# Kernel tuning notes

Hardware: AMD Instinct MI355X
Metric: run time of the kernel (lower is better)

The kernel has to match this reference:

```python
import jax, jax.numpy as jnp
import numpy as np
import math
from jax import lax

ROT = math.radians(45.0)   # rotation_range in radians
TR = 1.0                   # translation_range
P = 50                     # n_particles
ITERS = 30                 # n_iterations
SUB = 256                  # fitness_subsample
MU = P // 2
C_SIGMA = 0.3
D_SIGMA = 1.0


def axis_angle_to_R(a):
    # a: [..., 3] -> [..., 3, 3] via Rodrigues' formula
    theta = jnp.linalg.norm(a, axis=-1, keepdims=True)
    axis = a / (theta + 1e-8)
    x, y, z = axis[..., 0], axis[..., 1], axis[..., 2]
    o = jnp.zeros_like(x)
    K = jnp.stack([jnp.stack([o, -z, y], -1),
                   jnp.stack([z, o, -x], -1),
                   jnp.stack([-y, x, o], -1)], -2)
    th = theta[..., None]
    I = jnp.eye(3, dtype=a.dtype)
    return I + jnp.sin(th) * K + (1.0 - jnp.cos(th)) * (K @ K)


def chamfer(x, y):
    # x: [M,S,3], y: [M,T,3] -> [M]; symmetric chamfer on squared NN distances
    d2 = (jnp.sum(x * x, -1)[:, :, None] + jnp.sum(y * y, -1)[:, None, :]
          - 2.0 * jnp.einsum('msd,mtd->mst', x, y))
    return jnp.min(d2, axis=2).mean(axis=1) + jnp.min(d2, axis=1).mean(axis=1)


def evaluate(src, tgt, positions):
    # src [B,S,3], tgt [B,T,3], positions [B,Pn,6] -> fitness [B,Pn]
    B, Pn, _ = positions.shape
    R = axis_angle_to_R(positions[..., :3])            # [B,Pn,3,3]
    t = positions[..., 3:]
    transformed = jnp.einsum('bnj,bpkj->bpnk', src, R) + t[:, :, None, :]
    x = transformed.reshape(B * Pn, -1, 3)
    y = jnp.broadcast_to(tgt[:, None], (B, Pn) + tgt.shape[1:]).reshape(B * Pn, -1, 3)
    return chamfer(x, y).reshape(B, Pn)


def clamp6(v):
    return jnp.concatenate([jnp.clip(v[..., :3], -ROT, ROT),
                            jnp.clip(v[..., 3:], -TR, TR)], axis=-1)


def run_cmaes(source, target, key):
    B, N, _ = source.shape
    M = target.shape[1]
    S = min(SUB, N)
    k1, k2, k3 = jax.random.split(key, 3)
    src = source[:, jax.random.permutation(k1, N)[:S], :] if S < N else source
    tgt = target[:, jax.random.permutation(k2, M)[:S], :] if S < M else target

    mean = jnp.zeros((B, 6), jnp.float32)
    sigma = jnp.concatenate([jnp.full((B, 3), ROT * 0.3, jnp.float32),
                             jnp.full((B, 3), TR * 0.3, jnp.float32)], axis=1)
    w = np.log(MU + 0.5) - np.log(np.arange(1, MU + 1))
    w = jnp.asarray(w / w.sum(), jnp.float32)       # [MU] recombination weights
    gbest_pos = mean
    gbest_fit = jnp.full((B,), jnp.inf, jnp.float32)

    def step(carry, k):
        mean, sigma, gbest_pos, gbest_fit = carry
        z = jax.random.normal(k, (B, P, 6), jnp.float32)
        off = clamp6(mean[:, None] + sigma[:, None] * z)        # [B,P,6]
        fit = evaluate(src, tgt, off)                            # [B,P]
        order = jnp.argsort(fit, axis=1)
        pidx = order[:, :MU]
        pz = jnp.take_along_axis(z, pidx[..., None], axis=1)     # [B,MU,6]
        ppos = jnp.take_along_axis(off, pidx[..., None], axis=1)
        mean_new = jnp.einsum('m,bmd->bd', w, ppos)
        mean_z = jnp.einsum('m,bmd->bd', w, pz)
        s = sigma * jnp.exp(C_SIGMA / D_SIGMA * (jnp.mean(jnp.abs(mean_z), -1, keepdims=True) - 1.0))
        s = jnp.concatenate([jnp.clip(s[:, :3], ROT * 0.01, ROT * 0.5),
                             jnp.clip(s[:, 3:], TR * 0.01, TR * 0.5)], axis=1)
        best_fit = jnp.take_along_axis(fit, order[:, :1], axis=1)[:, 0]
        best_pos = jnp.take_along_axis(off, order[:, :1, None], axis=1)[:, 0]
        impr = best_fit < gbest_fit
        gbest_pos = jnp.where(impr[:, None], best_pos, gbest_pos)
        gbest_fit = jnp.where(impr, best_fit, gbest_fit)
        return (mean_new, s, gbest_pos, gbest_fit), None

    keys = jax.random.split(k3, ITERS)
    (mean, sigma, gbest_pos, gbest_fit), _ = lax.scan(step, (mean, sigma, gbest_pos, gbest_fit), keys)

    mean_fit = evaluate(src, tgt, mean[:, None, :])[:, 0]
    gbest_pos = jnp.where((mean_fit < gbest_fit)[:, None], mean, gbest_pos)
    return gbest_pos


def _forward(source, target):
    # Optimization runs under no_grad in the original -> stop_gradient here
    gbest = lax.stop_gradient(run_cmaes(source, target, jax.random.key(42)))
    R = axis_angle_to_R(gbest[:, :3])          # [B,3,3]
    t = gbest[:, 3:]                            # [B,3]
    aligned = jnp.einsum('bnj,bkj->bnk', source, R) + t[:, None, :]
    return R, t, aligned


def setup_inputs() -> dict:
    key = jax.random.key(0)
    k1, k2 = jax.random.split(key)
    source = jax.random.normal(k1, (32, 16384, 3), jnp.float32)
    target = jax.random.normal(k2, (32, 16384, 3), jnp.float32)
    return {"source": source, "target": target}


def reference(source, target):
    return _forward(source, target)
```

## Files before the change

### kernel.cpp

```cpp
#include <hip/hip_runtime.h>
#include <stdint.h>
#include <math.h>

#define NB 32
#define NPTS 16384
#define SS 256
#define POPP 50
#define MUU 25
#define NITERS 30

#define ROTF  ((float)0.7853981633974483)
#define SIG0R ((float)(0.7853981633974483*0.3))
#define SIG0T ((float)0.3)
#define SLOR  ((float)(0.7853981633974483*0.01))
#define SHIR  ((float)(0.7853981633974483*0.5))
#define SLOT  ((float)0.01)
#define SHIT  ((float)0.5)
#define SQRT2F ((float)1.4142135623730951)
#define ULOW  (-0.99999994f)

__host__ __device__ inline uint32_t rotl32(uint32_t v, int n){ return (v<<n)|(v>>(32-n)); }

__host__ __device__ inline void tf2x32(uint32_t k0, uint32_t k1, uint32_t x0, uint32_t x1,
                                       uint32_t &o0, uint32_t &o1){
  uint32_t ks2 = k0 ^ k1 ^ 0x1BD11BDAu;
  x0 += k0; x1 += k1;
#define TFR(r) { x0 += x1; x1 = rotl32(x1, r); x1 ^= x0; }
  TFR(13) TFR(15) TFR(26) TFR(6)
  x0 += k1; x1 += ks2 + 1u;
  TFR(17) TFR(29) TFR(16) TFR(24)
  x0 += ks2; x1 += k0 + 2u;
  TFR(13) TFR(15) TFR(26) TFR(6)
  x0 += k0; x1 += k1 + 3u;
  TFR(17) TFR(29) TFR(16) TFR(24)
  x0 += k1; x1 += ks2 + 4u;
  TFR(13) TFR(15) TFR(26) TFR(6)
  x0 += ks2; x1 += k0 + 5u;
#undef TFR
  o0 = x0; o1 = x1;
}

__device__ inline float erfinv32(float x){
  float w = -log1pf(-x*x);
  float p;
  if (w < 5.0f) {
    w = w - 2.5f;
    p = 2.81022636e-08f;
    p = fmaf(p, w, 3.43273939e-07f);
    p = fmaf(p, w, -3.5233877e-06f);
    p = fmaf(p, w, -4.39150654e-06f);
    p = fmaf(p, w, 0.00021858087f);
    p = fmaf(p, w, -0.00125372503f);
    p = fmaf(p, w, -0.00417768164f);
    p = fmaf(p, w, 0.246640727f);
    p = fmaf(p, w, 1.50140941f);
  } else {
    w = sqrtf(w) - 3.0f;
    p = -0.000200214257f;
    p = fmaf(p, w, 0.000100950558f);
    p = fmaf(p, w, 0.00134934322f);
    p = fmaf(p, w, -0.00367342844f);
    p = fmaf(p, w, 0.00573950773f);
    p = fmaf(p, w, -0.0076224613f);
    p = fmaf(p, w, 0.00943887047f);
    p = fmaf(p, w, 1.00167406f);
    p = fmaf(p, w, 2.83297682f);
  }
  return p * x;
}

__device__ inline void axisangle_R(float ax, float ay, float az, float R[9]){
  float th = sqrtf(ax*ax + ay*ay + az*az);
  float den = th + 1e-8f;
  float ux = ax/den, uy = ay/den, uz = az/den;
  float s = sinf(th), c = cosf(th);
  float omc = 1.0f - c;
  float xx=ux*ux, yy=uy*uy, zz=uz*uz;
  float xy=ux*uy, xz=ux*uz, yz=uy*uz;
  R[0] = 1.0f + omc*(-(yy+zz));
  R[1] = s*(-uz) + omc*xy;
  R[2] = s*uy    + omc*xz;
  R[3] = s*uz    + omc*xy;
  R[4] = 1.0f + omc*(-(xx+zz));
  R[5] = s*(-ux) + omc*yz;
  R[6] = s*(-uy) + omc*xz;
  R[7] = s*ux    + omc*yz;
  R[8] = 1.0f + omc*(-(xx+yy));
}

struct WArr { float w[MUU]; };

__global__ void k_init(float* mean, float* sigma, float* gbest_pos, float* gbest_fit){
  int i = blockIdx.x*blockDim.x + threadIdx.x;
  if (i < NB*6){
    mean[i] = 0.0f;
    gbest_pos[i] = 0.0f;
    int d = i % 6;
    sigma[i] = (d < 3) ? SIG0R : SIG0T;
  }
  if (i < NB) gbest_fit[i] = INFINITY;
}

__global__ void k_genperm(uint64_t* comp, uint32_t sa0, uint32_t sa1,
                          uint32_t sb0, uint32_t sb1, int round){
  int i = blockIdx.x*blockDim.x + threadIdx.x;
  if (i >= 2*NPTS) return;
  int a = i >> 14;
  int idx = i & (NPTS-1);
  uint32_t kk0 = a ? sb0 : sa0;
  uint32_t kk1 = a ? sb1 : sa1;
  uint32_t o0,o1; tf2x32(kk0, kk1, 0u, (uint32_t)idx, o0, o1);
  uint32_t key = o0 ^ o1;
  uint64_t val = (round == 0) ? (uint64_t)idx : (comp[i] & 0x3FFFull);
  comp[i] = ((uint64_t)key << 28) | ((uint64_t)idx << 14) | val;
}

__global__ __launch_bounds__(1024) void k_sort_local(uint64_t* comp){
  __shared__ uint64_t buf[4096];
  int c = blockIdx.x;
  int base = c * 4096;
  int abase = (c & 3) * 4096;
  for (int t = threadIdx.x; t < 4096; t += 1024) buf[t] = comp[base + t];
  __syncthreads();
  for (int k = 2; k <= 4096; k <<= 1){
    for (int j = k >> 1; j > 0; j >>= 1){
      for (int idx = threadIdx.x; idx < 2048; idx += 1024){
        int i = ((idx & ~(j-1)) << 1) | (idx & (j-1));
        int pi = i | j;
        bool dir = (((abase + i) & k) == 0);
        uint64_t A = buf[i], Bv = buf[pi];
        bool sw = dir ? (A > Bv) : (A < Bv);
        if (sw){ buf[i] = Bv; buf[pi] = A; }
      }
      __syncthreads();
    }
  }
  for (int t = threadIdx.x; t < 4096; t += 1024) comp[base + t] = buf[t];
}

__global__ void k_sort_global(uint64_t* comp, int k, int j){
  int t = blockIdx.x*blockDim.x + threadIdx.x;
  if (t >= NPTS) return;
  int a = t >> 13;
  int idx = t & 8191;
  int i = ((idx & ~(j-1)) << 1) | (idx & (j-1));
  int pi = i | j;
  bool dir = ((i & k) == 0);
  uint64_t* arr = comp + (size_t)a * NPTS;
  uint64_t A = arr[i], Bv = arr[pi];
  bool sw = dir ? (A > Bv) : (A < Bv);
  if (sw){ arr[i] = Bv; arr[pi] = A; }
}

__global__ __launch_bounds__(1024) void k_sort_finish(uint64_t* comp, int k){
  __shared__ uint64_t buf[4096];
  int c = blockIdx.x;
  int base = c * 4096;
  int abase = (c & 3) * 4096;
  for (int t = threadIdx.x; t < 4096; t += 1024) buf[t] = comp[base + t];
  __syncthreads();
  for (int j = 2048; j > 0; j >>= 1){
    for (int idx = threadIdx.x; idx < 2048; idx += 1024){
      int i = ((idx & ~(j-1)) << 1) | (idx & (j-1));
      int pi = i | j;
      bool dir = (((abase + i) & k) == 0);
      uint64_t A = buf[i], Bv = buf[pi];
      bool sw = dir ? (A > Bv) : (A < Bv);
      if (sw){ buf[i] = Bv; buf[pi] = A; }
    }
    __syncthreads();
  }
  for (int t = threadIdx.x; t < 4096; t += 1024) comp[base + t] = buf[t];
}

__global__ void k_gather(const uint64_t* comp, const float* source, const float* target,
                         float* src_sub, float* tgt_sub){
  int t = blockIdx.x*blockDim.x + threadIdx.x;
  if (t >= 2*NB*SS) return;
  int a = t / (NB*SS);
  int r = t % (NB*SS);
  int b = r / SS;
  int s2 = r % SS;
  int val = (int)(comp[(size_t)a*NPTS + s2] & 0x3FFFull);
  const float* inp = a ? target : source;
  float* outp = a ? tgt_sub : src_sub;
  for (int d = 0; d < 3; ++d)
    outp[((size_t)b*SS + s2)*3 + d] = inp[((size_t)b*NPTS + val)*3 + d];
}

__global__ __launch_bounds__(256) void k_se(uint32_t ka, uint32_t kb,
    const float* __restrict__ mean, const float* __restrict__ sigma,
    const float* __restrict__ src_sub, const float* __restrict__ tgt_sub,
    float* __restrict__ z_buf, float* __restrict__ off_buf,
    float* __restrict__ fit){
  int c = blockIdx.x;
  int b = c / POPP;
  int tid = threadIdx.x;
  int wave = tid >> 6;
  int lane = tid & 63;
  __shared__ float qoff[6];
  __shared__ float4 ysd[SS];
  __shared__ float4 xsd[SS];
  __shared__ float rmp[4][SS];
  __shared__ float cmp[4][SS];
  __shared__ float wpart[4];

  if (tid < 6){
    int i = c*6 + tid;
    uint32_t o0,o1; tf2x32(ka, kb, 0u, (uint32_t)i, o0, o1);
    uint32_t bits = o0 ^ o1;
    float u = __uint_as_float((bits >> 9) | 0x3F800000u) - 1.0f;
    u = u * 2.0f + ULOW;
    u = fmaxf(ULOW, u);
    float zz = SQRT2F * erfinv32(u);
    float m = mean[b*6 + tid], sg = sigma[b*6 + tid];
    float v = fmaf(sg, zz, m);
    float lim = (tid < 3) ? ROTF : 1.0f;
    v = fminf(fmaxf(v, -lim), lim);
    z_buf[i] = zz; off_buf[i] = v; qoff[tid] = v;
  }
  __syncthreads();

  float R[9];
  axisangle_R(qoff[0], qoff[1], qoff[2], R);
  float tx=qoff[3], ty=qoff[4], tz=qoff[5];

  {
    const float* tp = tgt_sub + ((size_t)b*SS + tid)*3;
    float Y0=tp[0], Y1=tp[1], Y2=tp[2];
    float sy = fmaf(Y2,Y2, fmaf(Y1,Y1, Y0*Y0));
    ysd[tid] = make_float4(-2.0f*Y0, -2.0f*Y1, -2.0f*Y2, sy);
  }
  {
    const float* sp = src_sub + ((size_t)b*SS + tid)*3;
    float X0=sp[0], X1=sp[1], X2=sp[2];
    float px = fmaf(X2, R[2], fmaf(X1, R[1], X0*R[0])) + tx;
    float py = fmaf(X2, R[5], fmaf(X1, R[4], X0*R[3])) + ty;
    float pz = fmaf(X2, R[8], fmaf(X1, R[7], X0*R[6])) + tz;
    float sx = fmaf(pz,pz, fmaf(py,py, px*px));
    xsd[tid] = make_float4(-2.0f*px, -2.0f*py, -2.0f*pz, sx);
  }
  __syncthreads();

  float pxj[4],pyj[4],pzj[4];
  float yxj[4],yyj[4],yzj[4];
  #pragma unroll
  for (int j = 0; j < 4; ++j){
    int i = lane + 64*j;
    float4 xv = xsd[i];
    pxj[j] = -0.5f*xv.x; pyj[j] = -0.5f*xv.y; pzj[j] = -0.5f*xv.z;
    float4 yv = ysd[i];
    yxj[j] = -0.5f*yv.x; yyj[j] = -0.5f*yv.y; yzj[j] = -0.5f*yv.z;
  }

  float rm0=INFINITY, rm1=INFINITY, rm2=INFINITY, rm3=INFINITY;
  float cm0=INFINITY, cm1=INFINITY, cm2=INFINITY, cm3=INFINITY;
  int tbeg = wave*64;
  #pragma unroll 8
  for (int t = tbeg; t < tbeg+64; ++t){
    float4 yv = ysd[t];
    float4 xv = xsd[t];
    rm0 = fminf(rm0, fmaf(pxj[0], yv.x, fmaf(pyj[0], yv.y, fmaf(pzj[0], yv.z, yv.w))));
    rm1 = fminf(rm1, fmaf(pxj[1], yv.x, fmaf(pyj[1], yv.y, fmaf(pzj[1], yv.z, yv.w))));
    rm2 = fminf(rm2, fmaf(pxj[2], yv.x, fmaf(pyj[2], yv.y, fmaf(pzj[2], yv.z, yv.w))));
    rm3 = fminf(rm3, fmaf(pxj[3], yv.x, fmaf(pyj[3], yv.y, fmaf(pzj[3], yv.z, yv.w))));
    cm0 = fminf(cm0, fmaf(yxj[0], xv.x, fmaf(yyj[0], xv.y, fmaf(yzj[0], xv.z, xv.w))));
    cm1 = fminf(cm1, fmaf(yxj[1], xv.x, fmaf(yyj[1], xv.y, fmaf(yzj[1], xv.z, xv.w))));
    cm2 = fminf(cm2, fmaf(yxj[2], xv.x, fmaf(yyj[2], xv.y, fmaf(yzj[2], xv.z, xv.w))));
    cm3 = fminf(cm3, fmaf(yxj[3], xv.x, fmaf(yyj[3], xv.y, fmaf(yzj[3], xv.z, xv.w))));
  }

  rmp[wave][lane+  0] = rm0;  cmp[wave][lane+  0] = cm0;
  rmp[wave][lane+ 64] = rm1;  cmp[wave][lane+ 64] = cm1;
  rmp[wave][lane+128] = rm2;  cmp[wave][lane+128] = cm2;
  rmp[wave][lane+192] = rm3;  cmp[wave][lane+192] = cm3;
  __syncthreads();

  float fx = xsd[tid].w + fminf(fminf(rmp[0][tid], rmp[1][tid]),
                                fminf(rmp[2][tid], rmp[3][tid]));
  float fy = ysd[tid].w + fminf(fminf(cmp[0][tid], cmp[1][tid]),
                                fminf(cmp[2][tid], cmp[3][tid]));
  float acc = fx + fy;

  for (int m = 32; m > 0; m >>= 1) acc += __shfl_xor(acc, m, 64);
  if (lane == 0) wpart[wave] = acc;
  __syncthreads();
  if (tid == 0) fit[c] = (((wpart[0]+wpart[1])+wpart[2])+wpart[3]) * (1.0f/256.0f);
}

__global__ __launch_bounds__(128) void k_eval(const float* __restrict__ pos, int Pn,
    const float* __restrict__ src_sub, const float* __restrict__ tgt_sub,
    float* __restrict__ fit){
  int c = blockIdx.x;
  int b = c / Pn;
  int tid = threadIdx.x;
  int wave = tid >> 6;
  int lane = tid & 63;
  __shared__ float4 ysd[SS];
  __shared__ float4 xsd[SS];
  __shared__ float wpart[2];

  const float* q = pos + (size_t)c*6;
  float R[9];
  axisangle_R(q[0], q[1], q[2], R);
  float tx=q[3], ty=q[4], tz=q[5];

  for (int i = tid; i < SS; i += 128){
    const float* tp = tgt_sub + ((size_t)b*SS + i)*3;
    float Y0=tp[0], Y1=tp[1], Y2=tp[2];
    float sy = fmaf(Y2,Y2, fmaf(Y1,Y1, Y0*Y0));
    ysd[i] = make_float4(-2.0f*Y0, -2.0f*Y1, -2.0f*Y2, sy);
  }

  int xi0 = wave*128 + lane;
  int xi1 = xi0 + 64;
  float px0,py0,pz0,sx0, px1,py1,pz1,sx1;
  {
    const float* sp = src_sub + ((size_t)b*SS + xi0)*3;
    float X0=sp[0], X1=sp[1], X2=sp[2];
    px0 = fmaf(X2, R[2], fmaf(X1, R[1], X0*R[0])) + tx;
    py0 = fmaf(X2, R[5], fmaf(X1, R[4], X0*R[3])) + ty;
    pz0 = fmaf(X2, R[8], fmaf(X1, R[7], X0*R[6])) + tz;
    sx0 = fmaf(pz0,pz0, fmaf(py0,py0, px0*px0));
    xsd[xi0] = make_float4(-2.0f*px0, -2.0f*py0, -2.0f*pz0, sx0);
  }
  {
    const float* sp = src_sub + ((size_t)b*SS + xi1)*3;
    float X0=sp[0], X1=sp[1], X2=sp[2];
    px1 = fmaf(X2, R[2], fmaf(X1, R[1], X0*R[0])) + tx;
    py1 = fmaf(X2, R[5], fmaf(X1, R[4], X0*R[3])) + ty;
    pz1 = fmaf(X2, R[8], fmaf(X1, R[7], X0*R[6])) + tz;
    sx1 = fmaf(pz1,pz1, fmaf(py1,py1, px1*px1));
    xsd[xi1] = make_float4(-2.0f*px1, -2.0f*py1, -2.0f*pz1, sx1);
  }
  __syncthreads();

  float rm0 = INFINITY, rm1 = INFINITY;
  #pragma unroll 8
  for (int t = 0; t < SS; ++t){
    float4 yv = ysd[t];
    rm0 = fminf(rm0, fmaf(px0, yv.x, fmaf(py0, yv.y, fmaf(pz0, yv.z, yv.w))));
    rm1 = fminf(rm1, fmaf(px1, yv.x, fmaf(py1, yv.y, fmaf(pz1, yv.z, yv.w))));
  }
  float acc = (sx0 + rm0) + (sx1 + rm1);

  float4 yv0 = ysd[xi0];
  float4 yv1 = ysd[xi1];
  float yx0 = -0.5f*yv0.x, yy0 = -0.5f*yv0.y, yz0 = -0.5f*yv0.z, sy0 = yv0.w;
  float yx1 = -0.5f*yv1.x, yy1 = -0.5f*yv1.y, yz1 = -0.5f*yv1.z, sy1 = yv1.w;
  float cm0 = INFINITY, cm1 = INFINITY;
  #pragma unroll 8
  for (int t = 0; t < SS; ++t){
    float4 xv = xsd[t];
    cm0 = fminf(cm0, fmaf(yx0, xv.x, fmaf(yy0, xv.y, fmaf(yz0, xv.z, xv.w))));
    cm1 = fminf(cm1, fmaf(yx1, xv.x, fmaf(yy1, xv.y, fmaf(yz1, xv.z, xv.w))));
  }
  acc += (sy0 + cm0) + (sy1 + cm1);

  for (int m = 32; m > 0; m >>= 1) acc += __shfl_xor(acc, m, 64);
  if (lane == 0) wpart[wave] = acc;
  __syncthreads();
  if (tid == 0) fit[c] = (wpart[0] + wpart[1]) * (1.0f/256.0f);
}

__global__ __launch_bounds__(64) void k_update(const float* __restrict__ fit,
    const float* __restrict__ off, const float* __restrict__ z,
    float* mean, float* sigma, float* gbest_pos, float* gbest_fit, WArr W){
  int b = blockIdx.x;
  int tid = threadIdx.x;
  __shared__ float lfit[POPP];
  __shared__ int order[POPP];
  __shared__ float mn[6], mz[6];
  if (tid < POPP) lfit[tid] = fit[b*POPP + tid];
  __syncthreads();
  if (tid < POPP){
    float f = lfit[tid];
    int r = 0;
    for (int j = 0; j < POPP; ++j){
      float fj = lfit[j];
      r += (fj < f) || (fj == f && j < tid);
    }
    order[r] = tid;
  }
  __syncthreads();
  if (tid < 6){
    float a = 0.0f, bz = 0.0f;
    for (int m = 0; m < MUU; ++m){
      int idx = order[m];
      a  = fmaf(W.w[m], off[((size_t)b*POPP + idx)*6 + tid], a);
      bz = fmaf(W.w[m], z  [((size_t)b*POPP + idx)*6 + tid], bz);
    }
    mn[tid] = a; mz[tid] = bz;
  }
  __syncthreads();
  if (tid == 0){
    float avg = (((((fabsf(mz[0])+fabsf(mz[1]))+fabsf(mz[2]))+fabsf(mz[3]))+fabsf(mz[4]))+fabsf(mz[5])) / 6.0f;
    float e = expf(0.3f * (avg - 1.0f));
    for (int d = 0; d < 6; ++d){
      float sN = sigma[b*6 + d] * e;
      float lo = (d < 3) ? SLOR : SLOT;
      float hi = (d < 3) ? SHIR : SHIT;
      sN = fminf(fmaxf(sN, lo), hi);
      sigma[b*6 + d] = sN;
      mean[b*6 + d] = mn[d];
    }
    int i0 = order[0];
    float bf = lfit[i0];
    if (bf < gbest_fit[b]){
      gbest_fit[b] = bf;
      for (int d = 0; d < 6; ++d) gbest_pos[b*6 + d] = off[((size_t)b*POPP + i0)*6 + d];
    }
  }
}

__global__ void k_finalize(const float* mean, const float* mean_fit,
                           const float* gbest_pos, const float* gbest_fit, float* out){
  int b = blockIdx.x;
  if (threadIdx.x != 0) return;
  bool um = mean_fit[b] < gbest_fit[b];
  float g[6];
  for (int d = 0; d < 6; ++d) g[d] = um ? mean[b*6 + d] : gbest_pos[b*6 + d];
  float R[9];
  axisangle_R(g[0], g[1], g[2], R);
  for (int i = 0; i < 9; ++i) out[b*9 + i] = R[i];
  for (int d = 0; d < 3; ++d) out[NB*9 + b*3 + d] = g[3 + d];
}

__global__ void k_aligned(const float* __restrict__ src, const float* __restrict__ out_rt,
                          float* __restrict__ aligned){
  int idx = blockIdx.x*blockDim.x + threadIdx.x;
  if (idx >= NB*NPTS) return;
  int b = idx / NPTS;
  const float* R = out_rt + b*9;
  const float* t = out_rt + NB*9 + b*3;
  const float* p = src + (size_t)idx*3;
  float X0=p[0], X1=p[1], X2=p[2];
  float* o = aligned + (size_t)idx*3;
  o[0] = fmaf(X2, R[2], fmaf(X1, R[1], X0*R[0])) + t[0];
  o[1] = fmaf(X2, R[5], fmaf(X1, R[4], X0*R[3])) + t[1];
  o[2] = fmaf(X2, R[8], fmaf(X1, R[7], X0*R[6])) + t[2];
}

struct HKey { uint32_t a, b; };
static inline HKey h_tf(HKey k, uint32_t x0, uint32_t x1){
  uint32_t o0,o1; tf2x32(k.a, k.b, x0, x1, o0, o1);
  return {o0, o1};
}

static void run_sort(uint64_t* comp, hipStream_t stream){
  hipLaunchKernelGGL(k_sort_local,  dim3(8),  dim3(1024), 0, stream, comp);
  hipLaunchKernelGGL(k_sort_global, dim3(64), dim3(256),  0, stream, comp, 8192, 4096);
  hipLaunchKernelGGL(k_sort_finish, dim3(8),  dim3(1024), 0, stream, comp, 8192);
  hipLaunchKernelGGL(k_sort_global, dim3(64), dim3(256),  0, stream, comp, 16384, 8192);
  hipLaunchKernelGGL(k_sort_global, dim3(64), dim3(256),  0, stream, comp, 16384, 4096);
  hipLaunchKernelGGL(k_sort_finish, dim3(8),  dim3(1024), 0, stream, comp, 16384);
}

extern "C" void kernel_launch(void* const* d_in, const int* in_sizes, int n_in,
                              void* d_out, int out_size, void* d_ws, size_t ws_size,
                              hipStream_t stream){
  const float* source = (const float*)d_in[0];
  const float* target = (const float*)d_in[1];
  float* out = (float*)d_out;

  uint8_t* w = (uint8_t*)d_ws;
  size_t o = 0;
  auto alloc = [&](size_t bytes){ void* p = w + o; o += (bytes + 255) & ~(size_t)255; return p; };
  uint64_t* comp   = (uint64_t*)alloc(2*(size_t)NPTS*8);
  float* src_sub   = (float*)alloc((size_t)NB*SS*3*4);
  float* tgt_sub   = (float*)alloc((size_t)NB*SS*3*4);
  float* z_buf     = (float*)alloc((size_t)NB*POPP*6*4);
  float* off_buf   = (float*)alloc((size_t)NB*POPP*6*4);
  float* fit_buf   = (float*)alloc((size_t)NB*POPP*4);
  float* mean_buf  = (float*)alloc((size_t)NB*6*4);
  float* sigma_buf = (float*)alloc((size_t)NB*6*4);
  float* gb_pos    = (float*)alloc((size_t)NB*6*4);
  float* gb_fit    = (float*)alloc((size_t)NB*4);
  float* mean_fit  = (float*)alloc((size_t)NB*4);
  (void)ws_size; (void)in_sizes; (void)n_in; (void)out_size;

  HKey key0 = {0u, 42u};
  HKey k1 = h_tf(key0, 0u, 0u);
  HKey k2 = h_tf(key0, 0u, 1u);
  HKey k3 = h_tf(key0, 0u, 2u);
  HKey srcA  = h_tf(k1, 0u, 0u);
  HKey srcS1 = h_tf(k1, 0u, 1u);
  HKey srcS2 = h_tf(srcA, 0u, 1u);
  HKey tgtA  = h_tf(k2, 0u, 0u);
  HKey tgtS1 = h_tf(k2, 0u, 1u);
  HKey tgtS2 = h_tf(tgtA, 0u, 1u);
  HKey itk[NITERS];
  for (int j = 0; j < NITERS; ++j) itk[j] = h_tf(k3, 0u, (uint32_t)j);

  WArr W;
  {
    double lw[MUU], s = 0.0;
    for (int m = 0; m < MUU; ++m){ lw[m] = log((double)MUU + 0.5) - log((double)(m+1)); s += lw[m]; }
    for (int m = 0; m < MUU; ++m) W.w[m] = (float)(lw[m] / s);
  }

  hipLaunchKernelGGL(k_init, dim3(1), dim3(256), 0, stream, mean_buf, sigma_buf, gb_pos, gb_fit);

  hipLaunchKernelGGL(k_genperm, dim3(128), dim3(256), 0, stream,
                     comp, srcS1.a, srcS1.b, tgtS1.a, tgtS1.b, 0);
  run_sort(comp, stream);
  hipLaunchKernelGGL(k_genperm, dim3(128), dim3(256), 0, stream,
                     comp, srcS2.a, srcS2.b, tgtS2.a, tgtS2.b, 1);
  run_sort(comp, stream);
  hipLaunchKernelGGL(k_gather, dim3(64), dim3(256), 0, stream,
                     comp, source, target, src_sub, tgt_sub);

  for (int it = 0; it < NITERS; ++it){
    hipLaunchKernelGGL(k_se, dim3(NB*POPP), dim3(256), 0, stream,
                       itk[it].a, itk[it].b, mean_buf, sigma_buf,
                       src_sub, tgt_sub, z_buf, off_buf, fit_buf);
    hipLaunchKernelGGL(k_update, dim3(NB), dim3(64), 0, stream,
                       fit_buf, off_buf, z_buf, mean_buf, sigma_buf, gb_pos, gb_fit, W);
  }

  hipLaunchKernelGGL(k_eval, dim3(NB), dim3(128), 0, stream,
                     mean_buf, 1, src_sub, tgt_sub, mean_fit);
  hipLaunchKernelGGL(k_finalize, dim3(NB), dim3(64), 0, stream,
                     mean_buf, mean_fit, gb_pos, gb_fit, out);
  hipLaunchKernelGGL(k_aligned, dim3((NB*NPTS + 255)/256), dim3(256), 0, stream,
                     source, out, out + NB*9 + NB*3);
}
```

Measured before the change: 950.0 us.

## Fuse CMA-ES update into sampling/eval kernel with ping-pong state buffers

The separate per-iteration k_update launch is removed. Each k_se block now redundantly recomputes the previous iteration's ranking, weighted mean, sigma adaptation and global-best update from double-buffered fitness, offset and z arrays before sampling its own particle. This halves the number of kernel launches in the 30-iteration loop, cutting launch and serialization overhead. In exchange, every block does a small rank-by-count sort and reduction, and all blocks of a batch race benignly to write identical mean, sigma and gbest values. A single trailing k_update applies the last iteration's update.

Result: faster. 893.2 us (-6.0%).

```diff
diff --git a/kernel.cpp b/kernel.cpp
--- a/kernel.cpp
+++ b/kernel.cpp
@@ -188,22 +188,87 @@
     outp[((size_t)b*SS + s2)*3 + d] = inp[((size_t)b*NPTS + val)*3 + d];
 }
 
-__global__ __launch_bounds__(256) void k_se(uint32_t ka, uint32_t kb,
-    const float* __restrict__ mean, const float* __restrict__ sigma,
+__global__ __launch_bounds__(256) void k_se(uint32_t ka, uint32_t kb, int it,
+    float* __restrict__ mean_base, float* __restrict__ sigma_base,
     const float* __restrict__ src_sub, const float* __restrict__ tgt_sub,
-    float* __restrict__ z_buf, float* __restrict__ off_buf,
-    float* __restrict__ fit){
+    float* __restrict__ z_base, float* __restrict__ off_base,
+    float* __restrict__ fit_base,
+    float* __restrict__ gb_pos, float* __restrict__ gb_fit, WArr W){
   int c = blockIdx.x;
   int b = c / POPP;
   int tid = threadIdx.x;
   int wave = tid >> 6;
   int lane = tid & 63;
+
+  int readP  = (it == 0) ? 0 : ((it-1)&1);
+  int writeP = it & 1;
+  const float* fitR = fit_base + readP*(NB*POPP);
+  float*       fitW = fit_base + writeP*(NB*POPP);
+  const float* zR   = z_base   + (size_t)readP*(NB*POPP*6);
+  float*       zC   = z_base   + (size_t)writeP*(NB*POPP*6);
+  const float* offR = off_base + (size_t)readP*(NB*POPP*6);
+  float*       offC = off_base + (size_t)writeP*(NB*POPP*6);
+  const float* sigR = sigma_base + readP*(NB*6);
+  float*       sigW = sigma_base + writeP*(NB*6);
+  const float* meanR = mean_base + readP*(NB*6);
+  float*       meanW = mean_base + writeP*(NB*6);
+
+  __shared__ float qmean[6], qsig[6];
+  __shared__ float lfit[POPP];
+  __shared__ int   order[POPP];
+  __shared__ float mn[6], mzs[6];
   __shared__ float qoff[6];
   __shared__ float4 ysd[SS];
   __shared__ float4 xsd[SS];
   __shared__ float rmp[4][SS];
   __shared__ float cmp[4][SS];
   __shared__ float wpart[4];
+
+  if (it > 0){
+    if (tid < POPP) lfit[tid] = fitR[b*POPP + tid];
+    __syncthreads();
+    if (tid < POPP){
+      float f = lfit[tid];
+      int r = 0;
+      for (int j = 0; j < POPP; ++j){
+        float fj = lfit[j];
+        r += (fj < f) || (fj == f && j < tid);
+      }
+      order[r] = tid;
+    }
+    __syncthreads();
+    if (tid < 6){
+      float a = 0.0f, bz = 0.0f;
+      for (int m = 0; m < MUU; ++m){
+        int idx = order[m];
+        a  = fmaf(W.w[m], offR[((size_t)b*POPP + idx)*6 + tid], a);
+        bz = fmaf(W.w[m], zR [((size_t)b*POPP + idx)*6 + tid], bz);
+      }
+      mn[tid] = a; mzs[tid] = bz;
+    }
+    __syncthreads();
+    if (tid == 0){
+      float avg = (((((fabsf(mzs[0])+fabsf(mzs[1]))+fabsf(mzs[2]))+fabsf(mzs[3]))+fabsf(mzs[4]))+fabsf(mzs[5])) / 6.0f;
+      float e = expf(0.3f * (avg - 1.0f));
+      for (int d = 0; d < 6; ++d){
+        float sN = sigR[b*6 + d] * e;
+        float lo = (d < 3) ? SLOR : SLOT;
+        float hi = (d < 3) ? SHIR : SHIT;
+        sN = fminf(fmaxf(sN, lo), hi);
+        qsig[d] = sN; sigW[b*6 + d] = sN;
+        qmean[d] = mn[d]; meanW[b*6 + d] = mn[d];
+      }
+      int i0 = order[0];
+      float bf = lfit[i0];
+      if (bf < gb_fit[b]){
+        gb_fit[b] = bf;
+        for (int d = 0; d < 6; ++d) gb_pos[b*6 + d] = offR[((size_t)b*POPP + i0)*6 + d];
+      }
+    }
+  } else {
+    if (tid < 6){ qmean[tid] = meanR[b*6 + tid]; qsig[tid] = sigR[b*6 + tid]; }
+  }
+  __syncthreads();
 
   if (tid < 6){
     int i = c*6 + tid;
@@ -213,11 +278,11 @@
     u = u * 2.0f + ULOW;
     u = fmaxf(ULOW, u);
     float zz = SQRT2F * erfinv32(u);
-    float m = mean[b*6 + tid], sg = sigma[b*6 + tid];
+    float m = qmean[tid], sg = qsig[tid];
     float v = fmaf(sg, zz, m);
     float lim = (tid < 3) ? ROTF : 1.0f;
     v = fminf(fmaxf(v, -lim), lim);
-    z_buf[i] = zz; off_buf[i] = v; qoff[tid] = v;
+    zC[i] = zz; offC[i] = v; qoff[tid] = v;
   }
   __syncthreads();
 
@@ -285,7 +350,7 @@
   for (int m = 32; m > 0; m >>= 1) acc += __shfl_xor(acc, m, 64);
   if (lane == 0) wpart[wave] = acc;
   __syncthreads();
-  if (tid == 0) fit[c] = (((wpart[0]+wpart[1])+wpart[2])+wpart[3]) * (1.0f/256.0f);
+  if (tid == 0) fitW[c] = (((wpart[0]+wpart[1])+wpart[2])+wpart[3]) * (1.0f/256.0f);
 }
 
 __global__ __launch_bounds__(128) void k_eval(const float* __restrict__ pos, int Pn,
@@ -469,11 +534,11 @@
   uint64_t* comp   = (uint64_t*)alloc(2*(size_t)NPTS*8);
   float* src_sub   = (float*)alloc((size_t)NB*SS*3*4);
   float* tgt_sub   = (float*)alloc((size_t)NB*SS*3*4);
-  float* z_buf     = (float*)alloc((size_t)NB*POPP*6*4);
-  float* off_buf   = (float*)alloc((size_t)NB*POPP*6*4);
-  float* fit_buf   = (float*)alloc((size_t)NB*POPP*4);
-  float* mean_buf  = (float*)alloc((size_t)NB*6*4);
-  float* sigma_buf = (float*)alloc((size_t)NB*6*4);
+  float* z_buf     = (float*)alloc(2*(size_t)NB*POPP*6*4);
+  float* off_buf   = (float*)alloc(2*(size_t)NB*POPP*6*4);
+  float* fit_buf   = (float*)alloc(2*(size_t)NB*POPP*4);
+  float* mean_buf  = (float*)alloc(2*(size_t)NB*6*4);
+  float* sigma_buf = (float*)alloc(2*(size_t)NB*6*4);
   float* gb_pos    = (float*)alloc((size_t)NB*6*4);
   float* gb_fit    = (float*)alloc((size_t)NB*4);
   float* mean_fit  = (float*)alloc((size_t)NB*4);
@@ -512,16 +577,19 @@
 
   for (int it = 0; it < NITERS; ++it){
     hipLaunchKernelGGL(k_se, dim3(NB*POPP), dim3(256), 0, stream,
-                       itk[it].a, itk[it].b, mean_buf, sigma_buf,
-                       src_sub, tgt_sub, z_buf, off_buf, fit_buf);
-    hipLaunchKernelGGL(k_update, dim3(NB), dim3(64), 0, stream,
-                       fit_buf, off_buf, z_buf, mean_buf, sigma_buf, gb_pos, gb_fit, W);
-  }
+                       itk[it].a, itk[it].b, it, mean_buf, sigma_buf,
+                       src_sub, tgt_sub, z_buf, off_buf, fit_buf,
+                       gb_pos, gb_fit, W);
+  }
+
+  hipLaunchKernelGGL(k_update, dim3(NB), dim3(64), 0, stream,
+                     fit_buf + NB*POPP, off_buf + (size_t)NB*POPP*6, z_buf + (size_t)NB*POPP*6,
+                     mean_buf + NB*6, sigma_buf + NB*6, gb_pos, gb_fit, W);
 
   hipLaunchKernelGGL(k_eval, dim3(NB), dim3(128), 0, stream,
-                     mean_buf, 1, src_sub, tgt_sub, mean_fit);
+                     mean_buf + NB*6, 1, src_sub, tgt_sub, mean_fit);
   hipLaunchKernelGGL(k_finalize, dim3(NB), dim3(64), 0, stream,
-                     mean_buf, mean_fit, gb_pos, gb_fit, out);
+                     mean_buf + NB*6, mean_fit, gb_pos, gb_fit, out);
   hipLaunchKernelGGL(k_aligned, dim3((NB*NPTS + 255)/256), dim3(256), 0, stream,
                      source, out, out + NB*9 + NB*3);
 }
```
